# Performance work log

Measured on AMD Instinct MI355X. Metric: run time of the kernel, lower is better.

Reference implementation:

```python
import jax, jax.numpy as jnp
import numpy as np

DIM_MODEL = 1024
NUM_HEADS = 16
HEAD_DIM = DIM_MODEL // NUM_HEADS


def setup_inputs() -> dict:
    key = jax.random.key(0)
    ks = jax.random.split(key, 10)
    B, S1, S2, D = 2, 1, 2048, DIM_MODEL
    q = jax.random.normal(ks[0], (B, S1, S2, 1, D), dtype=jnp.float32)
    k = jax.random.normal(ks[1], (B, S1, S2, 1, D), dtype=jnp.float32)
    v = jax.random.normal(ks[2], (B, S1, S2, 1, D), dtype=jnp.float32)
    mask = jnp.zeros((1,), dtype=jnp.bool_)
    inv_scale_factor = jnp.ones((1, 1, 1, 1), dtype=jnp.float32)
    s = 1.0 / np.sqrt(D)
    Wq = jax.random.uniform(ks[3], (D, D), jnp.float32, -s, s)
    bq = jax.random.uniform(ks[4], (D,), jnp.float32, -s, s)
    Wk = jax.random.uniform(ks[5], (D, D), jnp.float32, -s, s)
    bk = jax.random.uniform(ks[6], (D,), jnp.float32, -s, s)
    Wv = jax.random.uniform(ks[7], (D, D), jnp.float32, -s, s)
    bv = jax.random.uniform(ks[8], (D,), jnp.float32, -s, s)
    return {"q": q, "k": k, "v": v, "mask": mask, "inv_scale_factor": inv_scale_factor,
            "Wq": Wq, "bq": bq, "Wk": Wk, "bk": bk, "Wv": Wv, "bv": bv}


def reference(q, k, v, mask, inv_scale_factor, Wq, bq, Wk, bk, Wv, bv):
    # q,k,v: [B, S1, S2, 1, D]; mask is unused (faithful to source forward)
    B, S1, S2, _, D = q.shape
    H, Dh = NUM_HEADS, HEAD_DIM

    def proj(x, W, b):
        # torch Linear: x @ W.T + b, then view -> heads, transpose(2,3)
        y = jnp.einsum('bgsod,ed->bgsoe', x, W) + b  # o==1 collapses in reshape
        return jnp.swapaxes(y.reshape(B, S1, S2, H, Dh), 2, 3)  # [B,S1,H,S2,Dh]

    qh = proj(q, Wq, bq) / jnp.sqrt(jnp.asarray(Dh, q.dtype))
    kh = proj(k, Wk, bk)
    vh = proj(v, Wv, bv)

    scores = jnp.einsum('bghsd,bghtd->bghst', qh, kh) / inv_scale_factor  # [B,S1,H,S2,S2]
    p = jax.nn.softmax(scores.astype(jnp.float32), axis=-1).astype(q.dtype)
    # dropout_p=0 (eval): identity
    out = jnp.einsum('bghst,bghtd->bghsd', p, vh)  # [B,S1,H,S2,Dh]
    out = out.reshape(B, S1, H, S2 * Dh)
    out = jnp.transpose(out, (0, 1, 3, 2))  # torch transpose(2,3)
    return out.reshape(B, S1, -1)
```

## Files before the change

kernel.cpp:

```cpp
#include <hip/hip_runtime.h>
#include <stdint.h>

typedef short bf16x8 __attribute__((ext_vector_type(8)));
typedef float f32x4 __attribute__((ext_vector_type(4)));

static __device__ __forceinline__ unsigned short f2bf(float f) {
  union { float f; uint32_t u; } c; c.f = f;
  uint32_t u = c.u;
  uint32_t r = (u + 0x7fffu + ((u >> 16) & 1u)) >> 16;
  return (unsigned short)r;
}

extern "C" __device__ float __ocml_exp2_f32(float);
static __device__ __forceinline__ float exp2_(float x) {
#if __has_builtin(__builtin_amdgcn_exp2f)
  return __builtin_amdgcn_exp2f(x);
#else
  return __ocml_exp2_f32(x);
#endif
}

__device__ __forceinline__ void gload_lds16(const void* g, void* l) {
  __builtin_amdgcn_global_load_lds((const __attribute__((address_space(1))) uint32_t*)g,
                                   (__attribute__((address_space(3))) uint32_t*)l, 16, 0, 0);
}

__global__ __launch_bounds__(256) void k_convert(
    const float* __restrict__ q, const float* __restrict__ k, const float* __restrict__ v,
    const float* __restrict__ Wq, const float* __restrict__ Wk, const float* __restrict__ Wv,
    unsigned short* __restrict__ Xb, unsigned short* __restrict__ Wb) {
  const int NX4 = 3145728;
  const int NW4 = 786432;
  int i = blockIdx.x * 256 + threadIdx.x;
  if (i >= NX4 + NW4) return;
  const float* src; unsigned short* dst; int off4;
  if (i < NX4) {
    int a = i >> 20; off4 = i & 1048575;
    src = (a == 0) ? q : (a == 1) ? k : v;
    dst = Xb + (size_t)a * 4194304;
  } else {
    int j = i - NX4;
    int a = j >> 18; off4 = j & 262143;
    src = (a == 0) ? Wq : (a == 1) ? Wk : Wv;
    dst = Wb + (size_t)a * 1048576;
  }
  float4 f = ((const float4*)src)[off4];
  uint32_t lo = (uint32_t)f2bf(f.x) | ((uint32_t)f2bf(f.y) << 16);
  uint32_t hi = (uint32_t)f2bf(f.z) | ((uint32_t)f2bf(f.w) << 16);
  ((uint2*)dst)[off4] = make_uint2(lo, hi);
}

__global__ __launch_bounds__(256) void k_proj(
    const unsigned short* __restrict__ Xb, const unsigned short* __restrict__ Wb,
    const float* __restrict__ bq, const float* __restrict__ bk, const float* __restrict__ bv,
    const float* __restrict__ inv_scale,
    unsigned short* __restrict__ Qh, unsigned short* __restrict__ Kh,
    unsigned short* __restrict__ VhT) {
  __shared__ __align__(16) unsigned short At[128 * 32];
  __shared__ __align__(16) unsigned short Bt[128 * 32];
  const int g = blockIdx.y;
  const int m0 = (blockIdx.x >> 3) * 128, n0 = (blockIdx.x & 7) * 128;
  const unsigned short* X = Xb + (size_t)g * 4194304;
  const unsigned short* W = Wb + (size_t)g * 1048576;
  const int tid = threadIdx.x;
  const int w = tid >> 6, lane = tid & 63;
  const int wr = w >> 1, wc = w & 1;
  const int lq = lane & 15, lg = lane >> 4;

  f32x4 acc[4][4];
#pragma unroll
  for (int a = 0; a < 4; a++)
#pragma unroll
    for (int b = 0; b < 4; b++) acc[a][b] = (f32x4){0.f, 0.f, 0.f, 0.f};

  for (int kt = 0; kt < 32; ++kt) {
#pragma unroll
    for (int p = 0; p < 2; ++p) {
      int i = (w * 2 + p) * 64 + lane;
      int row = i >> 2, c = i & 3;
      gload_lds16(X + (size_t)(m0 + row) * 1024 + kt * 32 + c * 8, (char*)At + i * 16);
      gload_lds16(W + (size_t)(n0 + row) * 1024 + kt * 32 + c * 8, (char*)Bt + i * 16);
    }
    __syncthreads();
    bf16x8 af[4], bfr[4];
#pragma unroll
    for (int mi = 0; mi < 4; mi++)
      af[mi] = *(const bf16x8*)((const char*)At + ((wr * 64 + mi * 16 + lq) * 64 + lg * 16));
#pragma unroll
    for (int ni = 0; ni < 4; ni++)
      bfr[ni] = *(const bf16x8*)((const char*)Bt + ((wc * 64 + ni * 16 + lq) * 64 + lg * 16));
#pragma unroll
    for (int mi = 0; mi < 4; mi++)
#pragma unroll
      for (int ni = 0; ni < 4; ni++)
        acc[mi][ni] = __builtin_amdgcn_mfma_f32_16x16x32_bf16(af[mi], bfr[ni], acc[mi][ni], 0, 0, 0);
    __syncthreads();
  }

  const float* bias = (g == 0) ? bq : (g == 1) ? bk : bv;
  const float scale = (g == 0) ? 0.125f * 1.4426950408889634f / inv_scale[0] : 1.0f;
#pragma unroll
  for (int ni = 0; ni < 4; ni++) {
    int col = n0 + wc * 64 + ni * 16 + lq;
    float bb = bias[col];
    int h = col >> 6, dh = col & 63;
#pragma unroll
    for (int mi = 0; mi < 4; mi++) {
#pragma unroll
      for (int r = 0; r < 4; r++) {
        int row = m0 + wr * 64 + mi * 16 + lg * 4 + r;
        int b = row >> 11, s2 = row & 2047;
        unsigned short bv16 = f2bf((acc[mi][ni][r] + bb) * scale);
        if (g == 0)
          Qh[(size_t)(b * 16 + h) * 131072 + (size_t)s2 * 64 + dh] = bv16;
        else if (g == 1)
          Kh[(size_t)(b * 16 + h) * 131072 + (size_t)s2 * 64 + dh] = bv16;
        else
          VhT[(size_t)((b * 16 + h) * 64 + dh) * 2048 + s2] = bv16;
      }
    }
  }
}

__global__ __launch_bounds__(256) void k_attn(
    const unsigned short* __restrict__ Qh, const unsigned short* __restrict__ Kh,
    const unsigned short* __restrict__ VhT, float* __restrict__ Ot) {
  __shared__ __align__(16) unsigned short Kt[2][64 * 64];
  __shared__ __align__(16) unsigned short Pl[4][32][72];
  const int n = blockIdx.x;
  const int xcd = n & 7, slot = n >> 3;
  const int bh = (xcd << 2) | (slot >> 4);
  const int qt = slot & 15;
  const int tid = threadIdx.x;
  const int w = tid >> 6, lane = tid & 63;
  const int lq = lane & 15, lg = lane >> 4;
  const int qbase = qt * 128 + w * 32;

  bf16x8 qf[2][2];
#pragma unroll
  for (int r = 0; r < 2; r++) {
    const unsigned short* qp = Qh + ((size_t)bh * 2048 + qbase + r * 16 + lq) * 64 + lg * 8;
    qf[r][0] = *(const bf16x8*)(qp);
    qf[r][1] = *(const bf16x8*)(qp + 32);
  }

  f32x4 ofr[4][2];
#pragma unroll
  for (int dt = 0; dt < 4; dt++)
#pragma unroll
    for (int r = 0; r < 2; r++) ofr[dt][r] = (f32x4){0.f, 0.f, 0.f, 0.f};
  float m[2] = {-INFINITY, -INFINITY}, l[2] = {0.f, 0.f};

  const unsigned short* kgbase = Kh + (size_t)bh * 131072;
  const unsigned short* vbase = VhT + ((size_t)bh * 64 + lq) * 2048 + lg * 8;

#pragma unroll
  for (int p = 0; p < 2; ++p) {
    int i = (w * 2 + p) * 64 + lane;
    int row = i >> 3, c = i & 7;
    int cs = c ^ (row & 7);
    gload_lds16(kgbase + (size_t)row * 64 + cs * 8, (char*)Kt[0] + i * 16);
  }
  __syncthreads();

  for (int kv = 0; kv < 32; ++kv) {
    const int k0 = kv * 64;
    const char* ktc = (const char*)Kt[kv & 1];

    bf16x8 vr[4][2];
#pragma unroll
    for (int dt = 0; dt < 4; dt++) {
      const unsigned short* vp = vbase + (size_t)(dt * 16) * 2048 + k0;
      vr[dt][0] = *(const bf16x8*)(vp);
      vr[dt][1] = *(const bf16x8*)(vp + 32);
    }

    if (kv < 31) {
      char* ktn = (char*)Kt[(kv & 1) ^ 1];
#pragma unroll
      for (int p = 0; p < 2; ++p) {
        int i = (w * 2 + p) * 64 + lane;
        int row = i >> 3, c = i & 7;
        int cs = c ^ (row & 7);
        gload_lds16(kgbase + (size_t)(k0 + 64 + row) * 64 + cs * 8, ktn + i * 16);
      }
    }

    f32x4 sf[4][2];
#pragma unroll
    for (int t4 = 0; t4 < 4; t4++) {
      int row = t4 * 16 + lq;
      int c0 = lg ^ (row & 7), c1 = (4 + lg) ^ (row & 7);
      bf16x8 ka = *(const bf16x8*)(ktc + row * 128 + c0 * 16);
      bf16x8 kc = *(const bf16x8*)(ktc + row * 128 + c1 * 16);
#pragma unroll
      for (int r = 0; r < 2; r++) {
        f32x4 z = (f32x4){0.f, 0.f, 0.f, 0.f};
        z = __builtin_amdgcn_mfma_f32_16x16x32_bf16(ka, qf[r][0], z, 0, 0, 0);
        z = __builtin_amdgcn_mfma_f32_16x16x32_bf16(kc, qf[r][1], z, 0, 0, 0);
        sf[t4][r] = z;
      }
    }

    float pmax[2];
#pragma unroll
    for (int r = 0; r < 2; r++) {
      float a0 = fmaxf(fmaxf(sf[0][r][0], sf[0][r][1]), fmaxf(sf[0][r][2], sf[0][r][3]));
      float a1 = fmaxf(fmaxf(sf[1][r][0], sf[1][r][1]), fmaxf(sf[1][r][2], sf[1][r][3]));
      float a2 = fmaxf(fmaxf(sf[2][r][0], sf[2][r][1]), fmaxf(sf[2][r][2], sf[2][r][3]));
      float a3 = fmaxf(fmaxf(sf[3][r][0], sf[3][r][1]), fmaxf(sf[3][r][2], sf[3][r][3]));
      float a = fmaxf(fmaxf(a0, a1), fmaxf(a2, a3));
      a = fmaxf(a, __shfl_xor(a, 16));
      a = fmaxf(a, __shfl_xor(a, 32));
      pmax[r] = a;
    }
    if (__any((pmax[0] > m[0] + 8.f) || (pmax[1] > m[1] + 8.f))) {
#pragma unroll
      for (int r = 0; r < 2; r++) {
        float mn = fmaxf(m[r], pmax[r]);
        float c = exp2_(m[r] - mn);
        m[r] = mn;
        l[r] *= c;
#pragma unroll
        for (int dt = 0; dt < 4; dt++) ofr[dt][r] *= c;
      }
    }
#pragma unroll
    for (int r = 0; r < 2; r++) {
      float ps = 0.f;
#pragma unroll
      for (int t4 = 0; t4 < 4; t4++) {
        float p0 = exp2_(sf[t4][r][0] - m[r]);
        float p1 = exp2_(sf[t4][r][1] - m[r]);
        float p2 = exp2_(sf[t4][r][2] - m[r]);
        float p3 = exp2_(sf[t4][r][3] - m[r]);
        ps += (p0 + p1) + (p2 + p3);
        uint32_t w0 = (uint32_t)f2bf(p0) | ((uint32_t)f2bf(p1) << 16);
        uint32_t w1 = (uint32_t)f2bf(p2) | ((uint32_t)f2bf(p3) << 16);
        uint64_t dw = (uint64_t)w0 | ((uint64_t)w1 << 32);
        __builtin_memcpy((char*)&Pl[w][r * 16 + lq][0] + t4 * 32 + lg * 8, &dw, 8);
      }
      ps += __shfl_xor(ps, 16);
      ps += __shfl_xor(ps, 32);
      l[r] += ps;
    }

    bf16x8 pf[2][2];
#pragma unroll
    for (int r = 0; r < 2; r++)
#pragma unroll
      for (int c = 0; c < 2; c++)
        __builtin_memcpy(&pf[r][c], (const char*)&Pl[w][r * 16 + lq][0] + c * 64 + lg * 16, 16);
    __builtin_amdgcn_s_setprio(1);
#pragma unroll
    for (int dt = 0; dt < 4; dt++) {
#pragma unroll
      for (int r = 0; r < 2; r++) {
        ofr[dt][r] = __builtin_amdgcn_mfma_f32_16x16x32_bf16(vr[dt][0], pf[r][0], ofr[dt][r], 0, 0, 0);
        ofr[dt][r] = __builtin_amdgcn_mfma_f32_16x16x32_bf16(vr[dt][1], pf[r][1], ofr[dt][r], 0, 0, 0);
      }
    }
    __builtin_amdgcn_s_setprio(0);

    __syncthreads();
  }

  float rl[2] = {1.0f / l[0], 1.0f / l[1]};
#pragma unroll
  for (int dt = 0; dt < 4; dt++)
#pragma unroll
    for (int r = 0; r < 2; r++) {
      f32x4 o = ofr[dt][r] * rl[r];
      size_t q = qbase + r * 16 + lq;
      *(f32x4*)(Ot + ((size_t)bh * 2048 + q) * 64 + dt * 16 + lg * 4) = o;
    }
}

__global__ __launch_bounds__(256) void k_tr(const float* __restrict__ Ot,
                                            float* __restrict__ out) {
  int u = blockIdx.x * 256 + threadIdx.x;
  int h4 = u & 3, dh = (u >> 2) & 63, s2 = (u >> 8) & 2047, b = u >> 19;
  size_t base = ((size_t)(b * 16 + h4 * 4) * 2048 + s2) * 64 + dh;
  float4 o;
  o.x = Ot[base];
  o.y = Ot[base + 131072];
  o.z = Ot[base + 262144];
  o.w = Ot[base + 393216];
  ((float4*)out)[u] = o;
}

extern "C" void kernel_launch(void* const* d_in, const int* in_sizes, int n_in,
                              void* d_out, int out_size, void* d_ws, size_t ws_size,
                              hipStream_t stream) {
  const float* q   = (const float*)d_in[0];
  const float* k   = (const float*)d_in[1];
  const float* v   = (const float*)d_in[2];
  const float* inv = (const float*)d_in[4];
  const float* Wq  = (const float*)d_in[5];
  const float* bq  = (const float*)d_in[6];
  const float* Wk  = (const float*)d_in[7];
  const float* bk  = (const float*)d_in[8];
  const float* Wv  = (const float*)d_in[9];
  const float* bv  = (const float*)d_in[10];

  char* ws = (char*)d_ws;
  unsigned short* Xb  = (unsigned short*)(ws);
  unsigned short* Wb  = (unsigned short*)(ws + 25165824);
  unsigned short* Qh  = (unsigned short*)(ws + 31457280);
  unsigned short* Kh  = (unsigned short*)(ws + 39845888);
  unsigned short* VhT = (unsigned short*)(ws + 48234496);
  float*          Ot  = (float*)(ws);

  k_convert<<<15360, 256, 0, stream>>>(q, k, v, Wq, Wk, Wv, Xb, Wb);
  k_proj<<<dim3(256, 3), 256, 0, stream>>>(Xb, Wb, bq, bk, bv, inv, Qh, Kh, VhT);
  k_attn<<<512, 256, 0, stream>>>(Qh, Kh, VhT, Ot);
  k_tr<<<4096, 256, 0, stream>>>(Ot, (float*)d_out);
}
```

Baseline: 145.5 us.

## Stage V tiles through double-buffered LDS and swizzle P buffer

V tiles are now prefetched with async global-to-LDS loads into a double buffer alongside K, replacing per-iteration direct global register loads. The P staging buffer drops its padding and uses an XOR swizzle to avoid bank conflicts. The bf16 packing switches to the hardware v_cvt_pk_bf16_f32 instruction, and launch bounds request two blocks per CU. This hides V load latency behind compute at the cost of more LDS use and register pressure limits.

```diff
diff --git a/kernel.cpp b/kernel.cpp
--- a/kernel.cpp
+++ b/kernel.cpp
@@ -18,6 +18,12 @@
 #else
   return __ocml_exp2_f32(x);
 #endif
+}
+
+static __device__ __forceinline__ uint32_t cvtpk_bf16(float a, float b) {
+  uint32_t r;
+  asm("v_cvt_pk_bf16_f32 %0, %1, %2" : "=v"(r) : "v"(a), "v"(b));
+  return r;
 }
 
 __device__ __forceinline__ void gload_lds16(const void* g, void* l) {
@@ -122,11 +128,12 @@
   }
 }
 
-__global__ __launch_bounds__(256) void k_attn(
+__global__ __launch_bounds__(256, 2) void k_attn(
     const unsigned short* __restrict__ Qh, const unsigned short* __restrict__ Kh,
     const unsigned short* __restrict__ VhT, float* __restrict__ Ot) {
   __shared__ __align__(16) unsigned short Kt[2][64 * 64];
-  __shared__ __align__(16) unsigned short Pl[4][32][72];
+  __shared__ __align__(16) unsigned short Vt[2][64 * 64];
+  __shared__ __align__(16) unsigned short Pl[4][32][64];
   const int n = blockIdx.x;
   const int xcd = n & 7, slot = n >> 3;
   const int bh = (xcd << 2) | (slot >> 4);
@@ -152,37 +159,33 @@
   float m[2] = {-INFINITY, -INFINITY}, l[2] = {0.f, 0.f};
 
   const unsigned short* kgbase = Kh + (size_t)bh * 131072;
-  const unsigned short* vbase = VhT + ((size_t)bh * 64 + lq) * 2048 + lg * 8;
+  const unsigned short* vgbase = VhT + (size_t)bh * 64 * 2048;
 
 #pragma unroll
   for (int p = 0; p < 2; ++p) {
-    int i = (w * 2 + p) * 64 + lane;
+    int i = p * 256 + tid;
     int row = i >> 3, c = i & 7;
     int cs = c ^ (row & 7);
     gload_lds16(kgbase + (size_t)row * 64 + cs * 8, (char*)Kt[0] + i * 16);
+    gload_lds16(vgbase + (size_t)row * 2048 + cs * 8, (char*)Vt[0] + i * 16);
   }
   __syncthreads();
 
   for (int kv = 0; kv < 32; ++kv) {
     const int k0 = kv * 64;
     const char* ktc = (const char*)Kt[kv & 1];
-
-    bf16x8 vr[4][2];
-#pragma unroll
-    for (int dt = 0; dt < 4; dt++) {
-      const unsigned short* vp = vbase + (size_t)(dt * 16) * 2048 + k0;
-      vr[dt][0] = *(const bf16x8*)(vp);
-      vr[dt][1] = *(const bf16x8*)(vp + 32);
-    }
+    const char* vtc = (const char*)Vt[kv & 1];
 
     if (kv < 31) {
       char* ktn = (char*)Kt[(kv & 1) ^ 1];
+      char* vtn = (char*)Vt[(kv & 1) ^ 1];
 #pragma unroll
       for (int p = 0; p < 2; ++p) {
-        int i = (w * 2 + p) * 64 + lane;
+        int i = p * 256 + tid;
         int row = i >> 3, c = i & 7;
         int cs = c ^ (row & 7);
         gload_lds16(kgbase + (size_t)(k0 + 64 + row) * 64 + cs * 8, ktn + i * 16);
+        gload_lds16(vgbase + (size_t)row * 2048 + (k0 + 64) + cs * 8, vtn + i * 16);
       }
     }
 
@@ -225,6 +228,7 @@
         for (int dt = 0; dt < 4; dt++) ofr[dt][r] *= c;
       }
     }
+
 #pragma unroll
     for (int r = 0; r < 2; r++) {
       float ps = 0.f;
@@ -235,10 +239,11 @@
         float p2 = exp2_(sf[t4][r][2] - m[r]);
         float p3 = exp2_(sf[t4][r][3] - m[r]);
         ps += (p0 + p1) + (p2 + p3);
-        uint32_t w0 = (uint32_t)f2bf(p0) | ((uint32_t)f2bf(p1) << 16);
-        uint32_t w1 = (uint32_t)f2bf(p2) | ((uint32_t)f2bf(p3) << 16);
+        uint32_t w0 = cvtpk_bf16(p0, p1);
+        uint32_t w1 = cvtpk_bf16(p2, p3);
         uint64_t dw = (uint64_t)w0 | ((uint64_t)w1 << 32);
-        __builtin_memcpy((char*)&Pl[w][r * 16 + lq][0] + t4 * 32 + lg * 8, &dw, 8);
+        int ch = (t4 * 2 + (lg >> 1)) ^ (lq & 7);
+        __builtin_memcpy((char*)&Pl[w][r * 16 + lq][0] + ch * 16 + (lg & 1) * 8, &dw, 8);
       }
       ps += __shfl_xor(ps, 16);
       ps += __shfl_xor(ps, 32);
@@ -249,15 +254,21 @@
 #pragma unroll
     for (int r = 0; r < 2; r++)
 #pragma unroll
-      for (int c = 0; c < 2; c++)
-        __builtin_memcpy(&pf[r][c], (const char*)&Pl[w][r * 16 + lq][0] + c * 64 + lg * 16, 16);
+      for (int c = 0; c < 2; c++) {
+        int ch = (c * 4 + lg) ^ (lq & 7);
+        __builtin_memcpy(&pf[r][c], (const char*)&Pl[w][r * 16 + lq][0] + ch * 16, 16);
+      }
     __builtin_amdgcn_s_setprio(1);
 #pragma unroll
     for (int dt = 0; dt < 4; dt++) {
+      int row = dt * 16 + lq;
+      int c0 = lg ^ (row & 7), c1 = (4 + lg) ^ (row & 7);
+      bf16x8 va = *(const bf16x8*)(vtc + row * 128 + c0 * 16);
+      bf16x8 vc = *(const bf16x8*)(vtc + row * 128 + c1 * 16);
 #pragma unroll
       for (int r = 0; r < 2; r++) {
-        ofr[dt][r] = __builtin_amdgcn_mfma_f32_16x16x32_bf16(vr[dt][0], pf[r][0], ofr[dt][r], 0, 0, 0);
-        ofr[dt][r] = __builtin_amdgcn_mfma_f32_16x16x32_bf16(vr[dt][1], pf[r][1], ofr[dt][r], 0, 0, 0);
+        ofr[dt][r] = __builtin_amdgcn_mfma_f32_16x16x32_bf16(va, pf[r][0], ofr[dt][r], 0, 0, 0);
+        ofr[dt][r] = __builtin_amdgcn_mfma_f32_16x16x32_bf16(vc, pf[r][1], ofr[dt][r], 0, 0, 0);
       }
     }
     __builtin_amdgcn_s_setprio(0);
```

Measured after the change: 129.8 us. 1.12x faster.
